# Optimization experiments

Hardware: AMD Instinct MI355X
Metric: run time of the kernel (lower is better)

Reference implementation:

```python
import jax, jax.numpy as jnp
import numpy as np

HIDDEN = 2048
HEADS = 16
HEAD_DIM = HIDDEN // HEADS
D_FF = 4 * HIDDEN
B, T = 2, 2048
LN_EPS = 1e-5


def setup_inputs() -> dict:
    key = jax.random.key(0)
    ks = jax.random.split(key, 12)
    s = 0.02
    x = jax.random.normal(ks[0], (B, T, HIDDEN), dtype=jnp.float32)
    # strict upper-triangular True == masked (causal)
    causal_mask = jnp.triu(jnp.ones((T, T), dtype=bool), k=1)
    # weights stored as [in, out] (equivalent to torch Linear weight.T)
    Wq = jax.random.normal(ks[1], (HIDDEN, HIDDEN), jnp.float32) * s
    Wk = jax.random.normal(ks[2], (HIDDEN, HIDDEN), jnp.float32) * s
    Wv = jax.random.normal(ks[3], (HIDDEN, HIDDEN), jnp.float32) * s
    Wo = jax.random.normal(ks[4], (HIDDEN, HIDDEN), jnp.float32) * s
    ln1_w = jnp.ones((HIDDEN,), jnp.float32)
    ln1_b = jnp.zeros((HIDDEN,), jnp.float32)
    ln2_w = jnp.ones((HIDDEN,), jnp.float32)
    ln2_b = jnp.zeros((HIDDEN,), jnp.float32)
    W1 = jax.random.normal(ks[5], (HIDDEN, D_FF), jnp.float32) * s
    b1 = jnp.zeros((D_FF,), jnp.float32)
    W2 = jax.random.normal(ks[6], (D_FF, HIDDEN), jnp.float32) * s
    b2 = jnp.zeros((HIDDEN,), jnp.float32)
    return dict(x=x, causal_mask=causal_mask, Wq=Wq, Wk=Wk, Wv=Wv, Wo=Wo,
                ln1_w=ln1_w, ln1_b=ln1_b, ln2_w=ln2_w, ln2_b=ln2_b,
                W1=W1, b1=b1, W2=W2, b2=b2)


def _layernorm(x, w, b):
    mu = jnp.mean(x, axis=-1, keepdims=True)
    var = jnp.mean(jnp.square(x - mu), axis=-1, keepdims=True)
    return (x - mu) * jax.lax.rsqrt(var + LN_EPS) * w + b


def reference(x, causal_mask, Wq, Wk, Wv, Wo, ln1_w, ln1_b, ln2_w, ln2_b, W1, b1, W2, b2):
    Bx, Tx, H = x.shape
    h = _layernorm(x, ln1_w, ln1_b)
    # [B, T, heads, head_dim] -> [B, heads, T, head_dim]
    q = (h @ Wq).reshape(Bx, Tx, HEADS, HEAD_DIM).transpose(0, 2, 1, 3)
    k = (h @ Wk).reshape(Bx, Tx, HEADS, HEAD_DIM).transpose(0, 2, 1, 3)
    v = (h @ Wv).reshape(Bx, Tx, HEADS, HEAD_DIM).transpose(0, 2, 1, 3)
    scale = 1.0 / jnp.sqrt(jnp.float32(HEAD_DIM))
    scores = jnp.einsum('bhqd,bhkd->bhqk', q, k) * scale  # [B, heads, T, T]
    scores = jnp.where(causal_mask, -jnp.inf, scores)
    attn = jax.nn.softmax(scores, axis=-1)
    out = jnp.einsum('bhqk,bhkd->bhqd', attn, v)  # [B, heads, T, head_dim]
    out = out.transpose(0, 2, 1, 3).reshape(Bx, Tx, H)
    x = x + out @ Wo
    h2 = _layernorm(x, ln2_w, ln2_b)
    mlp = jax.nn.silu(h2 @ W1 + b1) @ W2 + b2
    return x + mlp
```

## Files before the change

### kernel.cpp

```cpp
#include <hip/hip_runtime.h>

#define HID 2048
#define NH 16
#define DH 128
#define DFF 8192
#define BB 2
#define TT 2048
#define MROWS 4096

typedef __bf16 bf16x8 __attribute__((ext_vector_type(8)));
typedef __bf16 bf16x4 __attribute__((ext_vector_type(4)));
typedef float  f32x4  __attribute__((ext_vector_type(4)));

__device__ __forceinline__ f32x4 mfma16(bf16x8 a, bf16x8 b, f32x4 c) {
    return __builtin_amdgcn_mfma_f32_16x16x32_bf16(a, b, c, 0, 0, 0);
}

__device__ __forceinline__ void gload_lds16(const __bf16* gsrc, __bf16* ldst) {
    __builtin_amdgcn_global_load_lds(
        (const __attribute__((address_space(1))) void*)gsrc,
        (__attribute__((address_space(3))) void*)ldst, 16, 0, 0);
}

template<int K, int N>
__global__ __launch_bounds__(256) void transpose_bf16_kernel(
    const float* __restrict__ W, __bf16* __restrict__ Wt) {
    __shared__ float tile[64][65];
    int tx = threadIdx.x;
    int ty = threadIdx.y;
    int n0 = blockIdx.x * 64;
    int k0 = blockIdx.y * 64;
    #pragma unroll
    for (int i = 0; i < 16; i++) {
        int kk = ty * 16 + i;
        tile[tx][kk] = W[(size_t)(k0 + kk) * N + n0 + tx];
    }
    __syncthreads();
    #pragma unroll
    for (int i = 0; i < 16; i++) {
        int nn = ty * 16 + i;
        Wt[(size_t)(n0 + nn) * K + k0 + tx] = (__bf16)tile[nn][tx];
    }
}

__global__ __launch_bounds__(256) void ln_kernel(
    const float* __restrict__ x, const float* __restrict__ gw,
    const float* __restrict__ gb, __bf16* __restrict__ out) {
    int row = blockIdx.x;
    int t = threadIdx.x;
    const float* xr = x + (size_t)row * HID;
    float4 v0 = *(const float4*)(xr + t * 8);
    float4 v1 = *(const float4*)(xr + t * 8 + 4);
    float xv[8] = {v0.x, v0.y, v0.z, v0.w, v1.x, v1.y, v1.z, v1.w};
    float s = 0.f, q = 0.f;
    #pragma unroll
    for (int j = 0; j < 8; j++) { s += xv[j]; q += xv[j] * xv[j]; }
    #pragma unroll
    for (int off = 1; off < 64; off <<= 1) {
        s += __shfl_xor(s, off);
        q += __shfl_xor(q, off);
    }
    __shared__ float ssum[4], ssq[4];
    if ((t & 63) == 0) { ssum[t >> 6] = s; ssq[t >> 6] = q; }
    __syncthreads();
    s = ssum[0] + ssum[1] + ssum[2] + ssum[3];
    q = ssq[0] + ssq[1] + ssq[2] + ssq[3];
    float mu = s * (1.0f / HID);
    float var = q * (1.0f / HID) - mu * mu;
    float rs = rsqrtf(var + 1e-5f);
    bf16x8 o;
    #pragma unroll
    for (int j = 0; j < 8; j++)
        o[j] = (__bf16)((xv[j] - mu) * rs * gw[t * 8 + j] + gb[t * 8 + j]);
    *(bf16x8*)(out + (size_t)row * HID + t * 8) = o;
}

template<int EPI, int BN, int BK, int N, int K>
__global__ __launch_bounds__(512) void gemm8(
    const __bf16* __restrict__ A, const __bf16* __restrict__ Bt,
    void* __restrict__ C0, void* __restrict__ C1, void* __restrict__ C2,
    const float* __restrict__ resid, const float* __restrict__ bias, int nN) {
    constexpr int BM = 256;
    constexpr int CPR = BK / 8;
    constexpr int RND_A = BM * BK * 2 / 8192;
    constexpr int RND_B = BN * BK * 2 / 8192;
    constexpr int LPT = RND_A + RND_B;
    constexpr int NT = K / BK;
    constexpr int WC = BN / 4;
    constexpr int NFRAG = WC / 16;
    constexpr int KK = BK / 32;

    __shared__ __align__(16) __bf16 As[3][BM * BK];
    __shared__ __align__(16) __bf16 Bs[3][BN * BK];

    int tid = threadIdx.x;
    int w = tid >> 6, l = tid & 63;
    int wr = w >> 2, wc = w & 3;
    int qi = l & 15, g = l >> 4;

    int nwg = gridDim.x;
    int bid = blockIdx.x;
    int wg = (bid & 7) * (nwg >> 3) + (bid >> 3);
    int bm = wg / nN, bn = wg % nN;
    int row0 = bm * BM, col0 = bn * BN;

    const __bf16* pA[RND_A];
    #pragma unroll
    for (int i = 0; i < RND_A; i++) {
        int slot = i * 512 + tid;
        int r = slot / CPR, u = slot % CPR;
        pA[i] = A + (size_t)(row0 + r) * K + (u ^ (r & (CPR - 1))) * 8;
    }
    const __bf16* pB[RND_B];
    #pragma unroll
    for (int i = 0; i < RND_B; i++) {
        int slot = i * 512 + tid;
        int r = slot / CPR, u = slot % CPR;
        pB[i] = Bt + (size_t)(col0 + r) * K + (u ^ (r & (CPR - 1))) * 8;
    }
    int wbase = w * 64 * 8;

    f32x4 acc[8][NFRAG] = {};

    #pragma unroll
    for (int tt = 0; tt < 2; tt++) {
        #pragma unroll
        for (int i = 0; i < RND_A; i++)
            gload_lds16(pA[i] + tt * BK, &As[tt][i * 4096 + wbase]);
        #pragma unroll
        for (int i = 0; i < RND_B; i++)
            gload_lds16(pB[i] + tt * BK, &Bs[tt][i * 4096 + wbase]);
    }

    __bf16 *a0 = As[0], *a1 = As[1], *a2 = As[2];
    __bf16 *b0 = Bs[0], *b1 = Bs[1], *b2 = Bs[2];

    for (int t = 0; t < NT; t++) {
        if constexpr (LPT == 6) asm volatile("s_waitcnt vmcnt(6)" ::: "memory");
        else                    asm volatile("s_waitcnt vmcnt(4)" ::: "memory");
        __builtin_amdgcn_s_barrier();
        asm volatile("" ::: "memory");
        if (t + 2 < NT) {
            #pragma unroll
            for (int i = 0; i < RND_A; i++)
                gload_lds16(pA[i] + (t + 2) * BK, a2 + i * 4096 + wbase);
            #pragma unroll
            for (int i = 0; i < RND_B; i++)
                gload_lds16(pB[i] + (t + 2) * BK, b2 + i * 4096 + wbase);
        }
        bf16x8 af[8][KK], bfr[NFRAG][KK];
        #pragma unroll
        for (int m = 0; m < 8; m++) {
            int r = wr * 128 + m * 16 + qi;
            #pragma unroll
            for (int kk = 0; kk < KK; kk++) {
                int byt = r * (BK * 2) + ((kk * 64 + g * 16) ^ ((r & (CPR - 1)) << 4));
                af[m][kk] = *(const bf16x8*)((const char*)a0 + byt);
            }
        }
        #pragma unroll
        for (int n = 0; n < NFRAG; n++) {
            int r = wc * WC + n * 16 + qi;
            #pragma unroll
            for (int kk = 0; kk < KK; kk++) {
                int byt = r * (BK * 2) + ((kk * 64 + g * 16) ^ ((r & (CPR - 1)) << 4));
                bfr[n][kk] = *(const bf16x8*)((const char*)b0 + byt);
            }
        }
        __builtin_amdgcn_s_setprio(1);
        #pragma unroll
        for (int kk = 0; kk < KK; kk++)
            #pragma unroll
            for (int m = 0; m < 8; m++)
                #pragma unroll
                for (int n = 0; n < NFRAG; n++)
                    acc[m][n] = mfma16(af[m][kk], bfr[n][kk], acc[m][n]);
        __builtin_amdgcn_s_setprio(0);
        asm volatile("" ::: "memory");
        __bf16* ta = a0; a0 = a1; a1 = a2; a2 = ta;
        __bf16* tb = b0; b0 = b1; b1 = b2; b2 = tb;
    }

    #pragma unroll
    for (int m = 0; m < 8; m++) {
        #pragma unroll
        for (int n = 0; n < NFRAG; n++) {
            int Rb = row0 + wr * 128 + m * 16 + g * 4;
            int C = col0 + wc * WC + n * 16 + qi;
            if constexpr (EPI == 6) {
                int region = C >> 11;
                int Cl = C & 2047;
                if (region < 2) {
                    __bf16* dst = (__bf16*)(region == 0 ? C0 : C1);
                    #pragma unroll
                    for (int r = 0; r < 4; r++)
                        dst[(size_t)(Rb + r) * 2048 + Cl] = (__bf16)acc[m][n][r];
                } else {
                    bf16x4 pk;
                    #pragma unroll
                    for (int r = 0; r < 4; r++) pk[r] = (__bf16)acc[m][n][r];
                    int b = Rb >> 11, t0 = Rb & 2047, hh = Cl >> 7, d = Cl & 127;
                    *(bf16x4*)((__bf16*)C2 + ((size_t)(b * NH + hh) * DH + d) * TT + t0) = pk;
                }
            } else {
                #pragma unroll
                for (int r = 0; r < 4; r++) {
                    int R = Rb + r;
                    float v = acc[m][n][r];
                    size_t idx = (size_t)R * N + C;
                    if constexpr (EPI == 0) {
                        ((__bf16*)C0)[idx] = (__bf16)v;
                    } else if constexpr (EPI == 2) {
                        ((float*)C0)[idx] = resid[idx] + v;
                    } else if constexpr (EPI == 3) {
                        float u = v + bias[C];
                        ((__bf16*)C0)[idx] = (__bf16)(u / (1.f + __expf(-u)));
                    } else if constexpr (EPI == 4) {
                        float u = v + bias[C];
                        ((float*)C0)[idx] = resid[idx] + u;
                    }
                }
            }
        }
    }
}

__global__ __launch_bounds__(256) void attn_kernel(
    const __bf16* __restrict__ qh, const __bf16* __restrict__ kh,
    const __bf16* __restrict__ vt, __bf16* __restrict__ out) {
    __shared__ __align__(16) __bf16 Ks[64 * 128];
    __shared__ __align__(16) __bf16 Vts[128 * 64];
    __shared__ __align__(16) __bf16 plds[4][1024];
    int tid = threadIdx.x;
    int w = tid >> 6, l = tid & 63;
    int qi = l & 15, g = l >> 4;
    int bh = blockIdx.y;
    int b = bh >> 4, hd = bh & 15;
    int qtile = gridDim.x - 1 - blockIdx.x;
    int qbase = qtile * 64 + w * 16;
    int qg = qbase + qi;

    const __bf16* qrow = qh + ((size_t)b * TT + qg) * HID + hd * DH;
    const __bf16* kbase = kh + (size_t)b * TT * HID + hd * DH;
    const __bf16* vtb = vt + (size_t)bh * DH * TT;

    bf16x8 bq[4];
    #pragma unroll
    for (int kc = 0; kc < 4; kc++)
        bq[kc] = *(const bf16x8*)(qrow + kc * 32 + g * 8);

    f32x4 O[8] = {};
    float m_run = -3.0e38f, l_run = 0.f;
    const float scale = 0.08838834764831845f;
    int nt = qtile + 1;

    for (int it = 0; it < nt; it++) {
        int kv0 = it * 64;
        __syncthreads();
        #pragma unroll
        for (int i = 0; i < 4; i++) {
            int j = (w * 4 + i) * 64 + l;
            int r = j >> 4, u = j & 15;
            int cb = (u * 16) ^ ((r & 7) << 4);
            gload_lds16(kbase + (size_t)(kv0 + r) * HID + (cb >> 1),
                        Ks + (w * 4 + i) * 512);
        }
        #pragma unroll
        for (int i = 0; i < 4; i++) {
            int j = (w * 4 + i) * 64 + l;
            int r = j >> 3, u = j & 7;
            int cb = (u * 16) ^ ((r & 7) << 4);
            gload_lds16(vtb + (size_t)r * TT + kv0 + (cb >> 1),
                        Vts + (w * 4 + i) * 512);
        }
        __syncthreads();

        f32x4 st[4] = {};
        #pragma unroll
        for (int t = 0; t < 4; t++) {
            #pragma unroll
            for (int kc = 0; kc < 4; kc++) {
                int row = t * 16 + qi;
                int cb = (kc * 64 + g * 16) ^ ((qi & 7) << 4);
                bf16x8 ak = *(const bf16x8*)(Ks + row * 128 + (cb >> 1));
                st[t] = mfma16(ak, bq[kc], st[t]);
            }
        }
        float s[16];
        #pragma unroll
        for (int t = 0; t < 4; t++)
            #pragma unroll
            for (int r = 0; r < 4; r++) s[t * 4 + r] = st[t][r] * scale;
        #pragma unroll
        for (int i = 0; i < 16; i++) {
            int kvg = kv0 + (i >> 2) * 16 + g * 4 + (i & 3);
            if (kvg > qg) s[i] = -3.0e38f;
        }
        float mt = s[0];
        #pragma unroll
        for (int i = 1; i < 16; i++) mt = fmaxf(mt, s[i]);
        mt = fmaxf(mt, __shfl_xor(mt, 16));
        mt = fmaxf(mt, __shfl_xor(mt, 32));
        float m_new = fmaxf(m_run, mt);
        float alpha = __expf(m_run - m_new);
        float p[16], ps = 0.f;
        #pragma unroll
        for (int i = 0; i < 16; i++) { p[i] = __expf(s[i] - m_new); ps += p[i]; }
        ps += __shfl_xor(ps, 16);
        ps += __shfl_xor(ps, 32);
        l_run = l_run * alpha + ps;
        m_run = m_new;

        #pragma unroll
        for (int t = 0; t < 4; t++) {
            bf16x4 pk;
            #pragma unroll
            for (int r = 0; r < 4; r++) pk[r] = (__bf16)p[t * 4 + r];
            int cb = (t * 32 + g * 8) ^ ((qi & 7) << 4);
            *(bf16x4*)(&plds[w][qi * 64 + (cb >> 1)]) = pk;
        }

        float av[4];
        #pragma unroll
        for (int r = 0; r < 4; r++) av[r] = __shfl(alpha, (g << 4) | (g * 4 + r));
        #pragma unroll
        for (int oc = 0; oc < 8; oc++)
            #pragma unroll
            for (int r = 0; r < 4; r++) O[oc][r] *= av[r];

        #pragma unroll
        for (int h = 0; h < 2; h++) {
            int cbp = (h * 64 + g * 16) ^ ((qi & 7) << 4);
            bf16x8 ap = *(const bf16x8*)(&plds[w][qi * 64 + (cbp >> 1)]);
            #pragma unroll
            for (int oc = 0; oc < 8; oc++) {
                int row = oc * 16 + qi;
                int cb = (h * 64 + g * 16) ^ ((qi & 7) << 4);
                bf16x8 bv = *(const bf16x8*)(Vts + row * 64 + (cb >> 1));
                O[oc] = mfma16(ap, bv, O[oc]);
            }
        }
    }

    float linv[4];
    #pragma unroll
    for (int r = 0; r < 4; r++) {
        float lq = __shfl(l_run, (g << 4) | (g * 4 + r));
        linv[r] = 1.0f / lq;
    }
    __bf16* op = out + ((size_t)b * TT + qbase) * HID + hd * DH;
    #pragma unroll
    for (int oc = 0; oc < 8; oc++)
        #pragma unroll
        for (int r = 0; r < 4; r++)
            op[(size_t)(g * 4 + r) * HID + oc * 16 + qi] = (__bf16)(O[oc][r] * linv[r]);
}

extern "C" void kernel_launch(void* const* d_in, const int* in_sizes, int n_in,
                              void* d_out, int out_size, void* d_ws, size_t ws_size,
                              hipStream_t stream) {
    const float* x    = (const float*)d_in[0];
    const float* Wq   = (const float*)d_in[2];
    const float* Wk   = (const float*)d_in[3];
    const float* Wv   = (const float*)d_in[4];
    const float* Wo   = (const float*)d_in[5];
    const float* ln1w = (const float*)d_in[6];
    const float* ln1b = (const float*)d_in[7];
    const float* ln2w = (const float*)d_in[8];
    const float* ln2b = (const float*)d_in[9];
    const float* W1   = (const float*)d_in[10];
    const float* b1   = (const float*)d_in[11];
    const float* W2   = (const float*)d_in[12];
    const float* b2   = (const float*)d_in[13];
    float* outp = (float*)d_out;

    char* ws = (char*)d_ws;
    const size_t SZ_W   = (size_t)HID * HID * 2;
    const size_t SZ_WF  = (size_t)HID * DFF * 2;
    const size_t SZ_ACT = (size_t)MROWS * HID * 2;
    const size_t SZ_X32 = (size_t)MROWS * HID * 4;

    __bf16* wqT  = (__bf16*)(ws);
    __bf16* wkT  = (__bf16*)(ws + SZ_W);
    __bf16* wvT  = (__bf16*)(ws + 2 * SZ_W);
    __bf16* woT  = (__bf16*)(ws + 3 * SZ_W);
    __bf16* w1T  = (__bf16*)(ws + 4 * SZ_W);
    __bf16* w2T  = (__bf16*)(ws + 4 * SZ_W + SZ_WF);
    __bf16* h    = (__bf16*)(ws + 4 * SZ_W + 2 * SZ_WF);
    float*  x1   = (float*) (ws + 4 * SZ_W + 2 * SZ_WF + SZ_ACT);
    char*   base = ws + 4 * SZ_W + 2 * SZ_WF + SZ_ACT + SZ_X32;
    __bf16* qb   = (__bf16*)(base);
    __bf16* kb   = (__bf16*)(base + SZ_ACT);
    __bf16* vtb  = (__bf16*)(base + 2 * SZ_ACT);
    __bf16* attn = (__bf16*)(base + 3 * SZ_ACT);
    __bf16* mlp1 = (__bf16*)(base);

    dim3 blk256(256), blk512(512);
    transpose_bf16_kernel<HID, HID><<<dim3(32, 32), dim3(64, 4), 0, stream>>>(Wq, wqT);
    transpose_bf16_kernel<HID, HID><<<dim3(32, 32), dim3(64, 4), 0, stream>>>(Wk, wkT);
    transpose_bf16_kernel<HID, HID><<<dim3(32, 32), dim3(64, 4), 0, stream>>>(Wv, wvT);
    transpose_bf16_kernel<HID, HID><<<dim3(32, 32), dim3(64, 4), 0, stream>>>(Wo, woT);
    transpose_bf16_kernel<HID, DFF><<<dim3(128, 32), dim3(64, 4), 0, stream>>>(W1, w1T);
    transpose_bf16_kernel<DFF, HID><<<dim3(32, 128), dim3(64, 4), 0, stream>>>(W2, w2T);

    ln_kernel<<<MROWS, blk256, 0, stream>>>(x, ln1w, ln1b, h);

    gemm8<6, 128, 64, 6144, HID><<<768, blk512, 0, stream>>>(
        h, wqT, qb, kb, vtb, nullptr, nullptr, 48);

    attn_kernel<<<dim3(TT / 64, BB * NH), blk256, 0, stream>>>(qb, kb, vtb, attn);

    gemm8<2, 128, 64, HID, HID><<<256, blk512, 0, stream>>>(
        attn, woT, x1, nullptr, nullptr, x, nullptr, 16);

    ln_kernel<<<MROWS, blk256, 0, stream>>>(x1, ln2w, ln2b, h);

    gemm8<3, 256, 32, DFF, HID><<<512, blk512, 0, stream>>>(
        h, w1T, mlp1, nullptr, nullptr, nullptr, b1, 32);
    gemm8<4, 128, 64, HID, DFF><<<256, blk512, 0, stream>>>(
        mlp1, w2T, outp, nullptr, nullptr, x1, b2, 16);
}
```

Baseline: 765.7 us.

## Vectorize weight transpose, raise MFMA wave priority, retile FFN1 GEMM

The weight-transpose kernel now reads float4 rows and writes bf16x4 vectors with a flat 256-thread block, where before it did scalar loads and stores. The attention kernel wraps its two MFMA loops in s_setprio(1)/s_setprio(0) so waves issuing matrix work get scheduling priority over waves doing softmax. The FFN1 GEMM switches from a 256x32 tile config to 128x64 with twice as many blocks. These are three unrelated tweaks: the transpose change cuts memory instructions, the priority hint targets overlap inside attention, and the retile changes occupancy and data reuse for the largest GEMM.

Measured after the change: 788.0 us. 1.03x slower.

```diff
diff --git a/kernel.cpp b/kernel.cpp
--- a/kernel.cpp
+++ b/kernel.cpp
@@ -26,20 +26,25 @@
 __global__ __launch_bounds__(256) void transpose_bf16_kernel(
     const float* __restrict__ W, __bf16* __restrict__ Wt) {
     __shared__ float tile[64][65];
-    int tx = threadIdx.x;
-    int ty = threadIdx.y;
-    int n0 = blockIdx.x * 64;
-    int k0 = blockIdx.y * 64;
-    #pragma unroll
-    for (int i = 0; i < 16; i++) {
-        int kk = ty * 16 + i;
-        tile[tx][kk] = W[(size_t)(k0 + kk) * N + n0 + tx];
+    int t = threadIdx.x;
+    int n0 = blockIdx.x * 64, k0 = blockIdx.y * 64;
+    int n4 = (t & 15) * 4, kk = t >> 4;
+    #pragma unroll
+    for (int i = 0; i < 4; i++) {
+        int k = i * 16 + kk;
+        float4 v = *(const float4*)(W + (size_t)(k0 + k) * N + n0 + n4);
+        tile[k][n4] = v.x; tile[k][n4 + 1] = v.y;
+        tile[k][n4 + 2] = v.z; tile[k][n4 + 3] = v.w;
     }
     __syncthreads();
-    #pragma unroll
-    for (int i = 0; i < 16; i++) {
-        int nn = ty * 16 + i;
-        Wt[(size_t)(n0 + nn) * K + k0 + tx] = (__bf16)tile[nn][tx];
+    int k4 = (t & 15) * 4, nn = t >> 4;
+    #pragma unroll
+    for (int i = 0; i < 4; i++) {
+        int n = i * 16 + nn;
+        bf16x4 o;
+        #pragma unroll
+        for (int j = 0; j < 4; j++) o[j] = (__bf16)tile[k4 + j][n];
+        *(bf16x4*)(Wt + (size_t)(n0 + n) * K + k0 + k4) = o;
     }
 }
 
@@ -276,6 +281,7 @@
         __syncthreads();
 
         f32x4 st[4] = {};
+        __builtin_amdgcn_s_setprio(1);
         #pragma unroll
         for (int t = 0; t < 4; t++) {
             #pragma unroll
@@ -286,6 +292,7 @@
                 st[t] = mfma16(ak, bq[kc], st[t]);
             }
         }
+        __builtin_amdgcn_s_setprio(0);
         float s[16];
         #pragma unroll
         for (int t = 0; t < 4; t++)
@@ -332,6 +339,7 @@
         for (int h = 0; h < 2; h++) {
             int cbp = (h * 64 + g * 16) ^ ((qi & 7) << 4);
             bf16x8 ap = *(const bf16x8*)(&plds[w][qi * 64 + (cbp >> 1)]);
+            __builtin_amdgcn_s_setprio(1);
             #pragma unroll
             for (int oc = 0; oc < 8; oc++) {
                 int row = oc * 16 + qi;
@@ -339,6 +347,7 @@
                 bf16x8 bv = *(const bf16x8*)(Vts + row * 64 + (cb >> 1));
                 O[oc] = mfma16(ap, bv, O[oc]);
             }
+            __builtin_amdgcn_s_setprio(0);
         }
     }
 
@@ -396,12 +405,12 @@
     __bf16* mlp1 = (__bf16*)(base);
 
     dim3 blk256(256), blk512(512);
-    transpose_bf16_kernel<HID, HID><<<dim3(32, 32), dim3(64, 4), 0, stream>>>(Wq, wqT);
-    transpose_bf16_kernel<HID, HID><<<dim3(32, 32), dim3(64, 4), 0, stream>>>(Wk, wkT);
-    transpose_bf16_kernel<HID, HID><<<dim3(32, 32), dim3(64, 4), 0, stream>>>(Wv, wvT);
-    transpose_bf16_kernel<HID, HID><<<dim3(32, 32), dim3(64, 4), 0, stream>>>(Wo, woT);
-    transpose_bf16_kernel<HID, DFF><<<dim3(128, 32), dim3(64, 4), 0, stream>>>(W1, w1T);
-    transpose_bf16_kernel<DFF, HID><<<dim3(32, 128), dim3(64, 4), 0, stream>>>(W2, w2T);
+    transpose_bf16_kernel<HID, HID><<<dim3(32, 32), blk256, 0, stream>>>(Wq, wqT);
+    transpose_bf16_kernel<HID, HID><<<dim3(32, 32), blk256, 0, stream>>>(Wk, wkT);
+    transpose_bf16_kernel<HID, HID><<<dim3(32, 32), blk256, 0, stream>>>(Wv, wvT);
+    transpose_bf16_kernel<HID, HID><<<dim3(32, 32), blk256, 0, stream>>>(Wo, woT);
+    transpose_bf16_kernel<HID, DFF><<<dim3(128, 32), blk256, 0, stream>>>(W1, w1T);
+    transpose_bf16_kernel<DFF, HID><<<dim3(32, 128), blk256, 0, stream>>>(W2, w2T);
 
     ln_kernel<<<MROWS, blk256, 0, stream>>>(x, ln1w, ln1b, h);
 
@@ -415,8 +424,9 @@
 
     ln_kernel<<<MROWS, blk256, 0, stream>>>(x1, ln2w, ln2b, h);
 
-    gemm8<3, 256, 32, DFF, HID><<<512, blk512, 0, stream>>>(
-        h, w1T, mlp1, nullptr, nullptr, nullptr, b1, 32);
+    gemm8<3, 128, 64, DFF, HID><<<1024, blk512, 0, stream>>>(
+        h, w1T, mlp1, nullptr, nullptr, nullptr, b1, 64);
+
     gemm8<4, 128, 64, HID, DFF><<<256, blk512, 0, stream>>>(
         mlp1, w2T, outp, nullptr, nullptr, x1, b2, 16);
 }
```
